# Kernel optimization log

Hardware: AMD Instinct MI355X
Metric: run time of the kernel (lower is better)

Reference implementation:

```python
import jax, jax.numpy as jnp
import numpy as np

N = 50000
E = 600000
D = 128


def setup_inputs() -> dict:
    key = jax.random.key(0)
    ks = jax.random.split(key, 6)
    x = jax.random.normal(ks[0], (N, D), dtype=jnp.float32)
    src = jax.random.randint(ks[1], (E,), 0, N, dtype=jnp.int32)
    dst = jax.random.randint(ks[2], (E,), 0, N, dtype=jnp.int32)
    W = jax.random.normal(ks[3], (D, D), dtype=jnp.float32) * (1.0 / np.sqrt(D))
    b = jax.random.normal(ks[4], (D,), dtype=jnp.float32) * 0.01
    root_emb = jax.random.normal(ks[5], (1, D), dtype=jnp.float32)
    return {"x": x, "src": src, "dst": dst, "W": W, "b": b, "root_emb": root_emb}


def reference(x, src, dst, W, b, root_emb):
    # h = Linear(x)
    h = x @ W.T + b  # (N, D)
    # in-degree (count of incoming edges per node) + 1 for self loop
    deg = jax.ops.segment_sum(jnp.ones((E,), dtype=jnp.float32), dst, num_segments=N) + 1.0  # (N,)
    deg_inv_sqrt = deg ** -0.5  # deg >= 1, no inf
    # per-edge symmetric norm
    norm = deg_inv_sqrt[src] * deg_inv_sqrt[dst]  # (E,)
    # message: norm * relu(h_src), scatter-sum to dst
    m = norm[:, None] * jax.nn.relu(h[src])  # (E, D)
    agg = jax.ops.segment_sum(m, dst, num_segments=N)  # (N, D)
    # self loop term
    self_loop = jax.nn.relu(h + root_emb) * (1.0 / deg)[:, None]
    return agg + self_loop
```

## Files before the change

kernel.cpp:

```cpp
#include <hip/hip_runtime.h>

#define DD 128

typedef _Float16 h8 __attribute__((ext_vector_type(8)));
typedef float f4 __attribute__((ext_vector_type(4)));

__global__ __launch_bounds__(256) void prep(const float* __restrict__ W,
    _Float16* __restrict__ Wh, int* __restrict__ cnt, int N) {
  const int gid = blockIdx.x * blockDim.x + threadIdx.x;
  const int stride = gridDim.x * blockDim.x;
  for (int i = gid; i < DD * DD; i += stride) Wh[i] = (_Float16)W[i];
  for (int i = gid; i < N; i += stride) cnt[i] = 0;
}

__global__ __launch_bounds__(256) void gemm_mfma(const float* __restrict__ x,
    const _Float16* __restrict__ Wh, const float* __restrict__ bias,
    _Float16* __restrict__ h16, const int* __restrict__ dst,
    int* __restrict__ cnt, int* __restrict__ slot, int E, int N) {
  __shared__ __align__(16) char lds[32768 + 32768 + 4096];
  const int tid = threadIdx.x;
  const int gid = blockIdx.x * 256 + tid;
  const int gsz = gridDim.x * 256;
  for (int e = gid; e < E; e += gsz) slot[e] = atomicAdd(cnt + dst[e], 1);

  const int lane = tid & 63;
  const int w    = tid >> 6;
  const int lrow = lane & 15;
  const int srow = (lane >> 4) << 2;
  const int row0 = blockIdx.x * 64;

#pragma unroll
  for (int i = 0; i < 8; ++i) {
    const char* s = (const char*)Wh + i * 4096 + tid * 16;
    __builtin_amdgcn_global_load_lds(
        (const __attribute__((address_space(1))) void*)s,
        (__attribute__((address_space(3))) void*)(lds + 32768 + i * 4096 + ((tid >> 6) << 10)),
        16, 0, 0);
  }
#pragma unroll
  for (int i = 0; i < 8; ++i) {
    const int ol = i * 4096 + tid * 16;
    const int r  = ol >> 9;
    const int cg = (ol >> 4) & 31;
    int grow = row0 + r; if (grow >= N) grow = N - 1;
    const char* s = (const char*)x + (size_t)grow * 512 + ((cg ^ (r & 7)) << 4);
    __builtin_amdgcn_global_load_lds(
        (const __attribute__((address_space(1))) void*)s,
        (__attribute__((address_space(3))) void*)(lds + i * 4096 + ((tid >> 6) << 10)),
        16, 0, 0);
  }
  __syncthreads();

  h8 wb[2][4];
  float bj[2];
#pragma unroll
  for (int jt = 0; jt < 2; ++jt) {
    const int col = w * 32 + jt * 16 + lrow;
    bj[jt] = bias[col];
#pragma unroll
    for (int ks = 0; ks < 4; ++ks)
      wb[jt][ks] = *(const h8*)(lds + 32768 + col * 256 + ks * 64 + (lane >> 4) * 16);
  }

  _Float16* cs = (_Float16*)(lds + 65536);
#pragma unroll
  for (int rt = 0; rt < 4; ++rt) {
    const int rowbase = row0 + rt * 16;
    if (rowbase >= N) break;
    f4 acc[2] = {(f4){0.f,0.f,0.f,0.f}, (f4){0.f,0.f,0.f,0.f}};
#pragma unroll
    for (int ks = 0; ks < 4; ++ks) {
      const int r   = rt * 16 + lrow;
      const int cg0 = ks * 8 + (lane >> 4) * 2;
      const f4 a0 = *(const f4*)(lds + r * 512 + ((cg0 ^ (r & 7)) << 4));
      const f4 a1 = *(const f4*)(lds + r * 512 + (((cg0 + 1) ^ (r & 7)) << 4));
      h8 af;
      af[0]=(_Float16)a0.x; af[1]=(_Float16)a0.y; af[2]=(_Float16)a0.z; af[3]=(_Float16)a0.w;
      af[4]=(_Float16)a1.x; af[5]=(_Float16)a1.y; af[6]=(_Float16)a1.z; af[7]=(_Float16)a1.w;
      acc[0] = __builtin_amdgcn_mfma_f32_16x16x32_f16(af, wb[0][ks], acc[0], 0, 0, 0);
      acc[1] = __builtin_amdgcn_mfma_f32_16x16x32_f16(af, wb[1][ks], acc[1], 0, 0, 0);
    }
#pragma unroll
    for (int jt = 0; jt < 2; ++jt)
#pragma unroll
      for (int r = 0; r < 4; ++r)
        cs[(srow + r) * DD + w * 32 + jt * 16 + lrow] = (_Float16)(acc[jt][r] + bj[jt]);
    __syncthreads();
    const int frow = rowbase + (tid >> 4);
    if (frow < N) {
      const f4 v = *(const f4*)((char*)cs + tid * 16);
      *(f4*)((char*)h16 + (size_t)frow * 256 + (tid & 15) * 16) = v;
    }
    __syncthreads();
  }
}

__global__ __launch_bounds__(256) void scan1(const int* __restrict__ cnt,
    int* __restrict__ rowptr, int* __restrict__ bsum, float* __restrict__ dis, int N) {
  __shared__ int s[256];
  const int tid = threadIdx.x;
  const int idx = blockIdx.x * 1024 + tid * 4;
  int4 v = {0, 0, 0, 0};
  if (idx + 3 < N) v = *(const int4*)(cnt + idx);
  else {
    if (idx + 0 < N) v.x = cnt[idx];
    if (idx + 1 < N) v.y = cnt[idx + 1];
    if (idx + 2 < N) v.z = cnt[idx + 2];
  }
  if (idx + 0 < N) dis[idx + 0] = rsqrtf((float)(v.x + 1));
  if (idx + 1 < N) dis[idx + 1] = rsqrtf((float)(v.y + 1));
  if (idx + 2 < N) dis[idx + 2] = rsqrtf((float)(v.z + 1));
  if (idx + 3 < N) dis[idx + 3] = rsqrtf((float)(v.w + 1));
  const int mysum = v.x + v.y + v.z + v.w;
  s[tid] = mysum;
  __syncthreads();
  for (int off = 1; off < 256; off <<= 1) {
    int t = (tid >= off) ? s[tid - off] : 0;
    __syncthreads();
    s[tid] += t;
    __syncthreads();
  }
  if (tid == 255) bsum[blockIdx.x] = s[255];
  int p = s[tid] - mysum;
  if (idx + 0 < N) rowptr[idx + 0] = p; p += v.x;
  if (idx + 1 < N) rowptr[idx + 1] = p; p += v.y;
  if (idx + 2 < N) rowptr[idx + 2] = p; p += v.z;
  if (idx + 3 < N) rowptr[idx + 3] = p;
}

__device__ __forceinline__ void boff_scan(const int* __restrict__ bsum,
    int* __restrict__ sbof, int tid, int nb) {
  if (tid < 64) {
    const int v = (tid < nb) ? bsum[tid] : 0;
    int incl = v;
#pragma unroll
    for (int off = 1; off < 64; off <<= 1) {
      const int t = __shfl_up(incl, off);
      if (tid >= off) incl += t;
    }
    sbof[tid] = incl - v;
  }
  __syncthreads();
}

__global__ __launch_bounds__(256) void fill_csr(const int* __restrict__ src,
    const int* __restrict__ dst, const int* __restrict__ rowptr,
    const int* __restrict__ bsum, const int* __restrict__ slot,
    int* __restrict__ esrc, int E, int nb) {
  __shared__ int sbof[64];
  const int tid = threadIdx.x;
  boff_scan(bsum, sbof, tid, nb);
  const int e4 = blockIdx.x * 256 + tid;
  const int e  = e4 * 4;
  if (e + 3 < E) {
    const int4 s4 = ((const int4*)src)[e4];
    const int4 d4 = ((const int4*)dst)[e4];
    const int4 l4 = ((const int4*)slot)[e4];
    esrc[rowptr[d4.x] + sbof[d4.x >> 10] + l4.x] = s4.x;
    esrc[rowptr[d4.y] + sbof[d4.y >> 10] + l4.y] = s4.y;
    esrc[rowptr[d4.z] + sbof[d4.z >> 10] + l4.z] = s4.z;
    esrc[rowptr[d4.w] + sbof[d4.w >> 10] + l4.w] = s4.w;
  } else if (e < E) {
    for (int i = e; i < E; ++i) {
      const int t = dst[i];
      esrc[rowptr[t] + sbof[t >> 10] + slot[i]] = src[i];
    }
  }
}

__global__ __launch_bounds__(256) void csr_agg(const int* __restrict__ esrc,
    const int* __restrict__ rowptr, const int* __restrict__ bsum,
    const _Float16* __restrict__ h16, const float* __restrict__ dis,
    const float* __restrict__ root, float* __restrict__ out, int N, int E, int nb) {
  __shared__ int sbof[64];
  const int tid = threadIdx.x;
  boff_scan(bsum, sbof, tid, nb);
  int gid = blockIdx.x * 256 + tid;
  if (gid >= N * 16) return;
  const int n = gid >> 4, q = gid & 15;
  const float dt  = dis[n];
  const float inv = dt * dt;
  const h8* hv8 = reinterpret_cast<const h8*>(h16);
  const f4 r0 = reinterpret_cast<const f4*>(root)[q * 2];
  const f4 r1 = reinterpret_cast<const f4*>(root)[q * 2 + 1];
  const h8 hv = hv8[n * 16 + q];
  float acc[8];
  acc[0] = fmaxf((float)hv[0] + r0.x, 0.0f) * inv;
  acc[1] = fmaxf((float)hv[1] + r0.y, 0.0f) * inv;
  acc[2] = fmaxf((float)hv[2] + r0.z, 0.0f) * inv;
  acc[3] = fmaxf((float)hv[3] + r0.w, 0.0f) * inv;
  acc[4] = fmaxf((float)hv[4] + r1.x, 0.0f) * inv;
  acc[5] = fmaxf((float)hv[5] + r1.y, 0.0f) * inv;
  acc[6] = fmaxf((float)hv[6] + r1.z, 0.0f) * inv;
  acc[7] = fmaxf((float)hv[7] + r1.w, 0.0f) * inv;
  float ea[8] = {0.f, 0.f, 0.f, 0.f, 0.f, 0.f, 0.f, 0.f};
  const int beg = rowptr[n] + sbof[n >> 10];
  const int end = (n == N - 1) ? E : rowptr[n + 1] + sbof[(n + 1) >> 10];
  int k = beg;
  for (; k + 3 < end; k += 4) {
    const int s0 = esrc[k], s1 = esrc[k + 1], s2 = esrc[k + 2], s3 = esrc[k + 3];
    const float w0 = dis[s0], w1 = dis[s1], w2 = dis[s2], w3 = dis[s3];
    const h8 g0 = hv8[s0 * 16 + q];
    const h8 g1 = hv8[s1 * 16 + q];
    const h8 g2 = hv8[s2 * 16 + q];
    const h8 g3 = hv8[s3 * 16 + q];
#pragma unroll
    for (int j = 0; j < 8; ++j)
      ea[j] += fmaxf((float)g0[j], 0.0f) * w0 + fmaxf((float)g1[j], 0.0f) * w1
             + fmaxf((float)g2[j], 0.0f) * w2 + fmaxf((float)g3[j], 0.0f) * w3;
  }
  for (; k < end; ++k) {
    const int s0 = esrc[k];
    const float w0 = dis[s0];
    const h8 g0 = hv8[s0 * 16 + q];
#pragma unroll
    for (int j = 0; j < 8; ++j) ea[j] += fmaxf((float)g0[j], 0.0f) * w0;
  }
  f4 o0, o1;
  o0.x = acc[0] + ea[0] * dt; o0.y = acc[1] + ea[1] * dt;
  o0.z = acc[2] + ea[2] * dt; o0.w = acc[3] + ea[3] * dt;
  o1.x = acc[4] + ea[4] * dt; o1.y = acc[5] + ea[5] * dt;
  o1.z = acc[6] + ea[6] * dt; o1.w = acc[7] + ea[7] * dt;
  reinterpret_cast<f4*>(out)[n * 32 + q * 2]     = o0;
  reinterpret_cast<f4*>(out)[n * 32 + q * 2 + 1] = o1;
}

extern "C" void kernel_launch(void* const* d_in, const int* in_sizes, int n_in,
                              void* d_out, int out_size, void* d_ws, size_t ws_size,
                              hipStream_t stream) {
  const float* x    = (const float*)d_in[0];
  const int*   src  = (const int*)d_in[1];
  const int*   dst  = (const int*)d_in[2];
  const float* W    = (const float*)d_in[3];
  const float* bias = (const float*)d_in[4];
  const float* root = (const float*)d_in[5];
  float* out = (float*)d_out;
  const int N = in_sizes[0] / DD;
  const int E = in_sizes[1];

  char* ws = (char*)d_ws;
  size_t off = 0;
  _Float16* h16 = (_Float16*)(ws + off); off += (size_t)N * DD * 2;
  int*   cnt    = (int*)  (ws + off); off += (size_t)N * 4;
  float* dis    = (float*)(ws + off); off += (size_t)N * 4;
  int*   rowptr = (int*)  (ws + off); off += (size_t)(N + 2) * 4;
  int*   esrc   = (int*)  (ws + off); off += (size_t)E * 4;
  int*   slot   = (int*)  (ws + off); off += (size_t)E * 4;
  int*   bsum   = (int*)  (ws + off); off += 256 * 4;
  _Float16* Wh  = (_Float16*)(ws + off); off += (size_t)DD * DD * 2;

  const int nb  = (N + 1023) / 1024;
  const int nbt = (N + 63) / 64;
  prep<<<128, 256, 0, stream>>>(W, Wh, cnt, N);
  gemm_mfma<<<nbt, 256, 0, stream>>>(x, Wh, bias, h16, dst, cnt, slot, E, N);
  scan1<<<nb, 256, 0, stream>>>(cnt, rowptr, bsum, dis, N);
  fill_csr<<<((E + 3) / 4 + 255) / 256, 256, 0, stream>>>(src, dst, rowptr, bsum, slot, esrc, E, nb);
  csr_agg<<<(N * 16 + 255) / 256, 256, 0, stream>>>(esrc, rowptr, bsum, h16, dis, root, out, N, E, nb);
}
```

Baseline: 86.14 us.

## Sort nodes by in-degree bucket to balance CSR aggregation wavefronts

Builds a degree histogram in scan1, turns it into bucket offsets in fill_csr, and adds a mkorder kernel that writes a node permutation grouped by in-degree. csr_agg then handles nodes in this order, so each wavefront holds nodes with similar edge counts and less divergence from uneven loop trip counts. The cost is an extra kernel launch, extra atomics, and scattered output writes and h16 self-reads because neighbouring threads no longer work on neighbouring nodes.

```diff
diff --git a/kernel.cpp b/kernel.cpp
--- a/kernel.cpp
+++ b/kernel.cpp
@@ -6,11 +6,12 @@
 typedef float f4 __attribute__((ext_vector_type(4)));
 
 __global__ __launch_bounds__(256) void prep(const float* __restrict__ W,
-    _Float16* __restrict__ Wh, int* __restrict__ cnt, int N) {
+    _Float16* __restrict__ Wh, int* __restrict__ cnt, int* __restrict__ ghist, int N) {
   const int gid = blockIdx.x * blockDim.x + threadIdx.x;
   const int stride = gridDim.x * blockDim.x;
   for (int i = gid; i < DD * DD; i += stride) Wh[i] = (_Float16)W[i];
   for (int i = gid; i < N; i += stride) cnt[i] = 0;
+  if (gid < 64) ghist[gid] = 0;
 }
 
 __global__ __launch_bounds__(256) void gemm_mfma(const float* __restrict__ x,
@@ -96,8 +97,10 @@
 }
 
 __global__ __launch_bounds__(256) void scan1(const int* __restrict__ cnt,
-    int* __restrict__ rowptr, int* __restrict__ bsum, float* __restrict__ dis, int N) {
+    int* __restrict__ rowptr, int* __restrict__ bsum, float* __restrict__ dis,
+    int* __restrict__ ghist, int N) {
   __shared__ int s[256];
+  __shared__ int lh[64];
   const int tid = threadIdx.x;
   const int idx = blockIdx.x * 1024 + tid * 4;
   int4 v = {0, 0, 0, 0};
@@ -107,6 +110,14 @@
     if (idx + 1 < N) v.y = cnt[idx + 1];
     if (idx + 2 < N) v.z = cnt[idx + 2];
   }
+  if (tid < 64) lh[tid] = 0;
+  __syncthreads();
+  if (idx + 0 < N) atomicAdd(&lh[min(v.x, 63)], 1);
+  if (idx + 1 < N) atomicAdd(&lh[min(v.y, 63)], 1);
+  if (idx + 2 < N) atomicAdd(&lh[min(v.z, 63)], 1);
+  if (idx + 3 < N) atomicAdd(&lh[min(v.w, 63)], 1);
+  __syncthreads();
+  if (tid < 64 && lh[tid]) atomicAdd(ghist + tid, lh[tid]);
   if (idx + 0 < N) dis[idx + 0] = rsqrtf((float)(v.x + 1));
   if (idx + 1 < N) dis[idx + 1] = rsqrtf((float)(v.y + 1));
   if (idx + 2 < N) dis[idx + 2] = rsqrtf((float)(v.z + 1));
@@ -146,9 +157,20 @@
 __global__ __launch_bounds__(256) void fill_csr(const int* __restrict__ src,
     const int* __restrict__ dst, const int* __restrict__ rowptr,
     const int* __restrict__ bsum, const int* __restrict__ slot,
-    int* __restrict__ esrc, int E, int nb) {
+    int* __restrict__ esrc, const int* __restrict__ ghist,
+    int* __restrict__ gcur, int E, int nb) {
   __shared__ int sbof[64];
   const int tid = threadIdx.x;
+  if (blockIdx.x == 0 && tid < 64) {
+    const int v = ghist[tid];
+    int incl = v;
+#pragma unroll
+    for (int off = 1; off < 64; off <<= 1) {
+      const int t = __shfl_up(incl, off);
+      if (tid >= off) incl += t;
+    }
+    gcur[tid] = incl - v;
+  }
   boff_scan(bsum, sbof, tid, nb);
   const int e4 = blockIdx.x * 256 + tid;
   const int e  = e4 * 4;
@@ -168,16 +190,45 @@
   }
 }
 
+__global__ __launch_bounds__(256) void mkorder(const int* __restrict__ cnt,
+    int* __restrict__ gcur, int* __restrict__ order, int N) {
+  __shared__ int lh[64], base[64];
+  const int tid = threadIdx.x;
+  if (tid < 64) lh[tid] = 0;
+  __syncthreads();
+  int bin[4], rk[4];
+  const int n0 = blockIdx.x * 1024 + tid * 4;
+#pragma unroll
+  for (int i = 0; i < 4; ++i) {
+    const int n = n0 + i;
+    if (n < N) {
+      bin[i] = min(cnt[n], 63);
+      rk[i] = atomicAdd(&lh[bin[i]], 1);
+    }
+  }
+  __syncthreads();
+  if (tid < 64) base[tid] = lh[tid] ? atomicAdd(&gcur[tid], lh[tid]) : 0;
+  __syncthreads();
+#pragma unroll
+  for (int i = 0; i < 4; ++i) {
+    const int n = n0 + i;
+    if (n < N) order[base[bin[i]] + rk[i]] = n;
+  }
+}
+
 __global__ __launch_bounds__(256) void csr_agg(const int* __restrict__ esrc,
     const int* __restrict__ rowptr, const int* __restrict__ bsum,
-    const _Float16* __restrict__ h16, const float* __restrict__ dis,
-    const float* __restrict__ root, float* __restrict__ out, int N, int E, int nb) {
+    const int* __restrict__ order, const _Float16* __restrict__ h16,
+    const float* __restrict__ dis, const float* __restrict__ root,
+    float* __restrict__ out, int N, int E, int nb) {
   __shared__ int sbof[64];
   const int tid = threadIdx.x;
   boff_scan(bsum, sbof, tid, nb);
-  int gid = blockIdx.x * 256 + tid;
-  if (gid >= N * 16) return;
-  const int n = gid >> 4, q = gid & 15;
+  const int gid = blockIdx.x * 256 + tid;
+  const bool alive = gid < N * 16;
+  const int g2 = alive ? gid : 0;
+  const int n = order[g2 >> 4];
+  const int q = g2 & 15;
   const float dt  = dis[n];
   const float inv = dt * dt;
   const h8* hv8 = reinterpret_cast<const h8*>(h16);
@@ -202,12 +253,12 @@
     const float w0 = dis[s0], w1 = dis[s1], w2 = dis[s2], w3 = dis[s3];
     const h8 g0 = hv8[s0 * 16 + q];
     const h8 g1 = hv8[s1 * 16 + q];
-    const h8 g2 = hv8[s2 * 16 + q];
+    const h8 g2v = hv8[s2 * 16 + q];
     const h8 g3 = hv8[s3 * 16 + q];
 #pragma unroll
     for (int j = 0; j < 8; ++j)
       ea[j] += fmaxf((float)g0[j], 0.0f) * w0 + fmaxf((float)g1[j], 0.0f) * w1
-             + fmaxf((float)g2[j], 0.0f) * w2 + fmaxf((float)g3[j], 0.0f) * w3;
+             + fmaxf((float)g2v[j], 0.0f) * w2 + fmaxf((float)g3[j], 0.0f) * w3;
   }
   for (; k < end; ++k) {
     const int s0 = esrc[k];
@@ -216,13 +267,15 @@
 #pragma unroll
     for (int j = 0; j < 8; ++j) ea[j] += fmaxf((float)g0[j], 0.0f) * w0;
   }
-  f4 o0, o1;
-  o0.x = acc[0] + ea[0] * dt; o0.y = acc[1] + ea[1] * dt;
-  o0.z = acc[2] + ea[2] * dt; o0.w = acc[3] + ea[3] * dt;
-  o1.x = acc[4] + ea[4] * dt; o1.y = acc[5] + ea[5] * dt;
-  o1.z = acc[6] + ea[6] * dt; o1.w = acc[7] + ea[7] * dt;
-  reinterpret_cast<f4*>(out)[n * 32 + q * 2]     = o0;
-  reinterpret_cast<f4*>(out)[n * 32 + q * 2 + 1] = o1;
+  if (alive) {
+    f4 o0, o1;
+    o0.x = acc[0] + ea[0] * dt; o0.y = acc[1] + ea[1] * dt;
+    o0.z = acc[2] + ea[2] * dt; o0.w = acc[3] + ea[3] * dt;
+    o1.x = acc[4] + ea[4] * dt; o1.y = acc[5] + ea[5] * dt;
+    o1.z = acc[6] + ea[6] * dt; o1.w = acc[7] + ea[7] * dt;
+    reinterpret_cast<f4*>(out)[n * 32 + q * 2]     = o0;
+    reinterpret_cast<f4*>(out)[n * 32 + q * 2 + 1] = o1;
+  }
 }
 
 extern "C" void kernel_launch(void* const* d_in, const int* in_sizes, int n_in,
@@ -246,14 +299,19 @@
   int*   rowptr = (int*)  (ws + off); off += (size_t)(N + 2) * 4;
   int*   esrc   = (int*)  (ws + off); off += (size_t)E * 4;
   int*   slot   = (int*)  (ws + off); off += (size_t)E * 4;
+  int*   order  = (int*)  (ws + off); off += (size_t)N * 4;
   int*   bsum   = (int*)  (ws + off); off += 256 * 4;
+  int*   ghist  = (int*)  (ws + off); off += 64 * 4;
+  int*   gcur   = (int*)  (ws + off); off += 64 * 4;
   _Float16* Wh  = (_Float16*)(ws + off); off += (size_t)DD * DD * 2;
 
   const int nb  = (N + 1023) / 1024;
   const int nbt = (N + 63) / 64;
-  prep<<<128, 256, 0, stream>>>(W, Wh, cnt, N);
+  const int nob = (N + 1023) / 1024;
+  prep<<<128, 256, 0, stream>>>(W, Wh, cnt, ghist, N);
   gemm_mfma<<<nbt, 256, 0, stream>>>(x, Wh, bias, h16, dst, cnt, slot, E, N);
-  scan1<<<nb, 256, 0, stream>>>(cnt, rowptr, bsum, dis, N);
-  fill_csr<<<((E + 3) / 4 + 255) / 256, 256, 0, stream>>>(src, dst, rowptr, bsum, slot, esrc, E, nb);
-  csr_agg<<<(N * 16 + 255) / 256, 256, 0, stream>>>(esrc, rowptr, bsum, h16, dis, root, out, N, E, nb);
-}
+  scan1<<<nb, 256, 0, stream>>>(cnt, rowptr, bsum, dis, ghist, N);
+  fill_csr<<<((E + 3) / 4 + 255) / 256, 256, 0, stream>>>(src, dst, rowptr, bsum, slot, esrc, ghist, gcur, E, nb);
+  mkorder<<<nob, 256, 0, stream>>>(cnt, gcur, order, N);
+  csr_agg<<<(N * 16 + 255) / 256, 256, 0, stream>>>(esrc, rowptr, bsum, order, h16, dis, root, out, N, E, nb);
+}
```

Result: slower. 89.76 us (+4.2%).
